# Optimization experiments

Measured on AMD Instinct MI355X. Metric: run time of the kernel, lower is better.

Reference implementation:

```python
import jax, jax.numpy as jnp
import numpy as np

# Complete 8-ary tree, depth 5 (levels 0..5), nodes stored level-major.
C = 8
DEPTH = 5
E = 64
H = 512
VOCAB = 20
SIZES = [C ** d for d in range(DEPTH + 1)]
OFFSETS = np.concatenate([[0], np.cumsum(SIZES)]).tolist()
TOTAL = OFFSETS[-1]  # 37449


def setup_inputs() -> dict:
    key = jax.random.key(0)
    ks = jax.random.split(key, 8)
    node_types = jax.random.randint(ks[0], (TOTAL,), 0, 19, dtype=jnp.int32)
    emb = jax.random.normal(ks[1], (VOCAB, E), jnp.float32)
    s_c = 1.0 / np.sqrt(E + H)
    s_g = 1.0 / np.sqrt(H)
    Wc_w = jax.random.normal(ks[2], (H, E + H), jnp.float32) * s_c
    Wc_b = jax.random.normal(ks[3], (H,), jnp.float32) * s_c
    W_ih = jax.random.normal(ks[4], (3 * H, H), jnp.float32) * s_g
    W_hh = jax.random.normal(ks[5], (3 * H, H), jnp.float32) * s_g
    b_ih = jax.random.normal(ks[6], (3 * H,), jnp.float32) * s_g
    b_hh = jax.random.normal(ks[7], (3 * H,), jnp.float32) * s_g
    return {"node_types": node_types, "emb": emb, "Wc_w": Wc_w, "Wc_b": Wc_b,
            "W_ih": W_ih, "W_hh": W_hh, "b_ih": b_ih, "b_hh": b_hh}


def _gru_last(seq, W_ih, W_hh, b_ih, b_hh):
    """PyTorch-convention GRU over child axis; seq: [n, C, H] -> last hidden [n, H]."""
    n = seq.shape[0]
    gx = jnp.einsum('ncH,gH->cng', seq, W_ih) + b_ih  # [C, n, 3H], precomputed input gates

    def step(h, gx_t):
        gh = h @ W_hh.T + b_hh
        xr, xz, xn = jnp.split(gx_t, 3, axis=-1)
        hr, hz, hn = jnp.split(gh, 3, axis=-1)
        r = jax.nn.sigmoid(xr + hr)
        z = jax.nn.sigmoid(xz + hz)
        cand = jnp.tanh(xn + r * hn)
        h_new = (1.0 - z) * cand + z * h
        return h_new, None

    h0 = jnp.zeros((n, H), seq.dtype)
    h_last, _ = jax.lax.scan(step, h0, gx)
    return h_last


def reference(node_types, emb, Wc_w, Wc_b, W_ih, W_hh, b_ih, b_hh):
    embeds = emb[node_types]                       # [TOTAL, E]
    Wc_e = Wc_w[:, :E]                              # acts on embedding part
    Wc_h = Wc_w[:, E:]                              # acts on child-encoding part
    # Leaf level: hidden part of concat is zero-padded -> only Wc_e contributes.
    off = OFFSETS[DEPTH]
    h = jnp.tanh(embeds[off:off + SIZES[DEPTH]] @ Wc_e.T + Wc_b)  # [8^5, H]
    # Bottom-up level batching: each internal node's children are contiguous.
    for d in range(DEPTH - 1, -1, -1):
        child_seq = h.reshape(SIZES[d], C, H)
        child_enc = _gru_last(child_seq, W_ih, W_hh, b_ih, b_hh)  # [8^d, H]
        off = OFFSETS[d]
        h = jnp.tanh(embeds[off:off + SIZES[d]] @ Wc_e.T + child_enc @ Wc_h.T + Wc_b)
    return h[0]  # root encoding, [H]
```

## Files before the change

kernel.cpp:

```cpp
#include <hip/hip_runtime.h>
#include <hip/hip_bf16.h>
#include <math.h>

#define HID 512
#define WCW_LD 576
#define LEAF 4681

typedef unsigned short u16;
typedef __attribute__((ext_vector_type(8))) short bf16x8;
typedef __attribute__((ext_vector_type(4))) float f32x4;

__device__ __forceinline__ u16 f2bf(float f) {
    union { float f; unsigned u; } x; x.f = f;
    unsigned r = x.u + 0x7fffu + ((x.u >> 16) & 1u);
    return (u16)(r >> 16);
}
__device__ __forceinline__ float bf2f(u16 b) {
    union { unsigned u; float f; } x; x.u = ((unsigned)b) << 16; return x.f;
}
__device__ __forceinline__ float sigm(float x) { return 1.f / (1.f + expf(-x)); }

__device__ __forceinline__ int swz(int row, int byte) { return byte ^ ((row & 7) << 4); }

__global__ void pe_kernel(const float* __restrict__ emb, const float* __restrict__ Wc_w,
                          const float* __restrict__ Wc_b, float* __restrict__ Pe,
                          u16* __restrict__ PeT16) {
    int v = blockIdx.x, j = threadIdx.x;
    __shared__ float e[64];
    if (threadIdx.x < 64) e[threadIdx.x] = emb[v * 64 + threadIdx.x];
    __syncthreads();
    float acc = Wc_b[j];
    const float* w = Wc_w + (long long)j * WCW_LD;
#pragma unroll 8
    for (int k = 0; k < 64; ++k) acc += e[k] * w[k];
    Pe[v * HID + j] = acc;
    PeT16[v * HID + j] = f2bf(tanhf(acc));
}

__global__ void conv_w_kernel(const float* __restrict__ W_ih, const float* __restrict__ W_hh,
                              const float* __restrict__ Wc_w,
                              u16* __restrict__ Wih16, u16* __restrict__ Whh16,
                              u16* __restrict__ Wch16) {
    int idx = blockIdx.x * blockDim.x + threadIdx.x;
    int stride = gridDim.x * blockDim.x;
    for (int i = idx; i < 3 * HID * HID; i += stride) {
        Wih16[i] = f2bf(W_ih[i]);
        Whh16[i] = f2bf(W_hh[i]);
    }
    for (int i = idx; i < HID * HID; i += stride) {
        int j = i >> 9, k = i & 511;
        Wch16[i] = f2bf(Wc_w[(long long)j * WCW_LD + 64 + k]);
    }
}

__global__ __launch_bounds__(256)
void gx20_kernel(const u16* __restrict__ PeT16, const u16* __restrict__ Wih16,
                 const float* __restrict__ b_ih, float* __restrict__ Gx20) {
    int v = blockIdx.x;
    int j = blockIdx.y * 256 + threadIdx.x;
    const u16* a = PeT16 + v * HID;
    const u16* b = Wih16 + (long long)j * HID;
    float acc = b_ih[j];
    for (int k = 0; k < HID; k += 8) {
        bf16x8 av = *(const bf16x8*)(a + k);
        bf16x8 bv = *(const bf16x8*)(b + k);
#pragma unroll
        for (int i = 0; i < 8; ++i) acc += bf2f((u16)av[i]) * bf2f((u16)bv[i]);
    }
    Gx20[v * 1536 + j] = acc;
}

__global__ void h1_kernel(const float* __restrict__ Gx20, const float* __restrict__ b_hh,
                          float* __restrict__ H1f, u16* __restrict__ H1_16) {
    int v = blockIdx.x, j = threadIdx.x;
    float xr = Gx20[v * 1536 + j], xz = Gx20[v * 1536 + 512 + j], xn = Gx20[v * 1536 + 1024 + j];
    float r = sigm(xr + b_hh[j]);
    float z = sigm(xz + b_hh[HID + j]);
    float cand = tanhf(xn + r * b_hh[2 * HID + j]);
    float h = (1.f - z) * cand;
    H1f[v * HID + j] = h;
    H1_16[v * HID + j] = f2bf(h);
}

__global__ __launch_bounds__(256)
void gx_gemm(const u16* __restrict__ Asrc, const u16* __restrict__ Wih16,
             const float* __restrict__ b_ih, u16* __restrict__ gx16, int M) {
    __shared__ __align__(16) uint8_t sA[128 * 128];
    __shared__ __align__(16) uint8_t sB[64 * 128];
    int tid = threadIdx.x, lane = tid & 63, w = tid >> 6;
    int j0 = blockIdx.x * 64;
    int m0 = blockIdx.y * 128;

    f32x4 acc[2][4];
#pragma unroll
    for (int m = 0; m < 2; ++m)
#pragma unroll
        for (int jf = 0; jf < 4; ++jf) acc[m][jf] = (f32x4){0.f, 0.f, 0.f, 0.f};

    for (int k0 = 0; k0 < HID; k0 += 64) {
#pragma unroll
        for (int l = 0; l < 4; ++l) {
            int e = tid + l * 256;
            int r = e >> 3, c = e & 7;
            int gm = m0 + r;
            uint4 v = make_uint4(0u, 0u, 0u, 0u);
            if (gm < M) v = *(const uint4*)(Asrc + (long long)gm * HID + k0 + c * 8);
            *(uint4*)(sA + r * 128 + swz(r, c * 16)) = v;
        }
#pragma unroll
        for (int l = 0; l < 2; ++l) {
            int e = tid + l * 256;
            int r = e >> 3, c = e & 7;
            uint4 v = *(const uint4*)(Wih16 + (long long)(j0 + r) * HID + k0 + c * 8);
            *(uint4*)(sB + r * 128 + swz(r, c * 16)) = v;
        }
        __syncthreads();
#pragma unroll
        for (int ks = 0; ks < 2; ++ks) {
            int kb = ks * 64 + ((lane >> 4) << 4);
            int ar = lane & 15;
            bf16x8 a0 = *(const bf16x8*)(sA + (w * 32 + ar) * 128 + swz(ar, kb));
            bf16x8 a1 = *(const bf16x8*)(sA + (w * 32 + 16 + ar) * 128 + swz(ar, kb));
#pragma unroll
            for (int jf = 0; jf < 4; ++jf) {
                bf16x8 b = *(const bf16x8*)(sB + (jf * 16 + ar) * 128 + swz(ar, kb));
                acc[0][jf] = __builtin_amdgcn_mfma_f32_16x16x32_bf16(a0, b, acc[0][jf], 0, 0, 0);
                acc[1][jf] = __builtin_amdgcn_mfma_f32_16x16x32_bf16(a1, b, acc[1][jf], 0, 0, 0);
            }
        }
        __syncthreads();
    }

#pragma unroll
    for (int jf = 0; jf < 4; ++jf) {
        int j = j0 + jf * 16 + (lane & 15);
        float bias = b_ih[j];
#pragma unroll
        for (int m = 0; m < 2; ++m) {
#pragma unroll
            for (int q = 0; q < 4; ++q) {
                int row = m0 + w * 32 + m * 16 + (lane >> 4) * 4 + q;
                if (row < M) gx16[(long long)row * 1536 + j] = f2bf(acc[m][jf][q] + bias);
            }
        }
    }
}

template<int GX_TABLE, int H_TABLE>
__global__ __launch_bounds__(256, 4)
void gru_step_h(const u16* __restrict__ hsrc16, const float* __restrict__ hsrc_f,
                const u16* __restrict__ H1_16, const float* __restrict__ H1f,
                const float* __restrict__ Gx20, const u16* __restrict__ gx16, int t,
                const int* __restrict__ nt,
                float* __restrict__ hdst_f, u16* __restrict__ hdst16,
                const u16* __restrict__ Whh16, const float* __restrict__ b_hh, int n) {
    __shared__ __align__(16) uint8_t sm[4][8192];
    int tid = threadIdx.x;
    int p0 = blockIdx.x * 64, j0 = blockIdx.y * 64;
    int lane = tid & 63, w = tid >> 6, wr = w >> 1, wc = w & 1;

    f32x4 acc[3][2][2];
#pragma unroll
    for (int g = 0; g < 3; ++g)
#pragma unroll
        for (int i = 0; i < 2; ++i)
#pragma unroll
            for (int j = 0; j < 2; ++j) acc[g][i][j] = (f32x4){0.f, 0.f, 0.f, 0.f};

    for (int kt = 0; kt < 8; ++kt) {
        int k0 = kt * 64;
#pragma unroll
        for (int l = 0; l < 2; ++l) {
            int e = tid + l * 256;
            int r = e >> 3, c = e & 7;
            int p = p0 + r;
            uint4 v = make_uint4(0u, 0u, 0u, 0u);
            if (p < n) {
                const u16* src = H_TABLE ? (H1_16 + (long long)nt[LEAF + p * 8] * HID)
                                         : (hsrc16 + (long long)p * HID);
                v = *(const uint4*)(src + k0 + c * 8);
            }
            *(uint4*)(sm[0] + r * 128 + swz(r, c * 16)) = v;
        }
#pragma unroll
        for (int g = 0; g < 3; ++g) {
#pragma unroll
            for (int l = 0; l < 2; ++l) {
                int e = tid + l * 256;
                int r = e >> 3, c = e & 7;
                uint4 v = *(const uint4*)(Whh16 + (long long)(g * HID + j0 + r) * HID + k0 + c * 8);
                *(uint4*)(sm[1 + g] + r * 128 + swz(r, c * 16)) = v;
            }
        }
        __syncthreads();
#pragma unroll
        for (int s = 0; s < 2; ++s) {
            int kb = s * 64 + ((lane >> 4) << 4);
            int ar = lane & 15;
            bf16x8 a0 = *(const bf16x8*)(sm[0] + (wr * 32 + ar) * 128 + swz(ar, kb));
            bf16x8 a1 = *(const bf16x8*)(sm[0] + (wr * 32 + 16 + ar) * 128 + swz(ar, kb));
#pragma unroll
            for (int g = 0; g < 3; ++g) {
#pragma unroll
                for (int jf = 0; jf < 2; ++jf) {
                    bf16x8 b = *(const bf16x8*)(sm[1 + g] + (wc * 32 + jf * 16 + ar) * 128 + swz(ar, kb));
                    acc[g][0][jf] = __builtin_amdgcn_mfma_f32_16x16x32_bf16(a0, b, acc[g][0][jf], 0, 0, 0);
                    acc[g][1][jf] = __builtin_amdgcn_mfma_f32_16x16x32_bf16(a1, b, acc[g][1][jf], 0, 0, 0);
                }
            }
        }
        __syncthreads();
    }

#pragma unroll
    for (int i = 0; i < 2; ++i) {
#pragma unroll
        for (int jf = 0; jf < 2; ++jf) {
            int jj = j0 + wc * 32 + jf * 16 + (lane & 15);
            float bhr = b_hh[jj], bhz = b_hh[HID + jj], bhn = b_hh[2 * HID + jj];
#pragma unroll
            for (int q = 0; q < 4; ++q) {
                int p = p0 + wr * 32 + i * 16 + (lane >> 4) * 4 + q;
                if (p >= n) continue;
                float xr, xz, xn;
                if (GX_TABLE) {
                    int v = nt[LEAF + p * 8 + t];
                    const float* gp = Gx20 + (long long)v * 1536 + jj;
                    xr = gp[0]; xz = gp[512]; xn = gp[1024];
                } else {
                    long long gb = ((long long)(p * 8 + t)) * 1536 + jj;
                    xr = bf2f(gx16[gb]); xz = bf2f(gx16[gb + 512]); xn = bf2f(gx16[gb + 1024]);
                }
                float hp = H_TABLE ? H1f[(long long)nt[LEAF + p * 8] * HID + jj]
                                   : hsrc_f[(long long)p * HID + jj];
                float r = sigm(xr + acc[0][i][jf][q] + bhr);
                float z = sigm(xz + acc[1][i][jf][q] + bhz);
                float cand = tanhf(xn + r * (acc[2][i][jf][q] + bhn));
                float hnew = (1.f - z) * cand + z * hp;
                hdst_f[(long long)p * HID + jj] = hnew;
                hdst16[(long long)p * HID + jj] = f2bf(hnew);
            }
        }
    }
}

__global__ __launch_bounds__(256, 4)
void combine_mfma(const u16* __restrict__ enc_in, const u16* __restrict__ Wch16,
                  const int* __restrict__ nt, int off, const float* __restrict__ Pe,
                  u16* __restrict__ out16, int n) {
    __shared__ __align__(16) uint8_t sm[2][8192];
    int tid = threadIdx.x;
    int p0 = blockIdx.x * 64, j0 = blockIdx.y * 64;
    int lane = tid & 63, w = tid >> 6, wr = w >> 1, wc = w & 1;

    f32x4 acc[2][2];
#pragma unroll
    for (int i = 0; i < 2; ++i)
#pragma unroll
        for (int j = 0; j < 2; ++j) acc[i][j] = (f32x4){0.f, 0.f, 0.f, 0.f};

    for (int kt = 0; kt < 8; ++kt) {
        int k0 = kt * 64;
#pragma unroll
        for (int l = 0; l < 2; ++l) {
            int e = tid + l * 256;
            int r = e >> 3, c = e & 7;
            uint4 v = make_uint4(0u, 0u, 0u, 0u);
            if (p0 + r < n) v = *(const uint4*)(enc_in + (long long)(p0 + r) * HID + k0 + c * 8);
            *(uint4*)(sm[0] + r * 128 + swz(r, c * 16)) = v;
        }
#pragma unroll
        for (int l = 0; l < 2; ++l) {
            int e = tid + l * 256;
            int r = e >> 3, c = e & 7;
            uint4 v = *(const uint4*)(Wch16 + (long long)(j0 + r) * HID + k0 + c * 8);
            *(uint4*)(sm[1] + r * 128 + swz(r, c * 16)) = v;
        }
        __syncthreads();
#pragma unroll
        for (int s = 0; s < 2; ++s) {
            int kb = s * 64 + ((lane >> 4) << 4);
            int ar = lane & 15;
            bf16x8 a0 = *(const bf16x8*)(sm[0] + (wr * 32 + ar) * 128 + swz(ar, kb));
            bf16x8 a1 = *(const bf16x8*)(sm[0] + (wr * 32 + 16 + ar) * 128 + swz(ar, kb));
#pragma unroll
            for (int j = 0; j < 2; ++j) {
                bf16x8 b = *(const bf16x8*)(sm[1] + (wc * 32 + j * 16 + ar) * 128 + swz(ar, kb));
                acc[0][j] = __builtin_amdgcn_mfma_f32_16x16x32_bf16(a0, b, acc[0][j], 0, 0, 0);
                acc[1][j] = __builtin_amdgcn_mfma_f32_16x16x32_bf16(a1, b, acc[1][j], 0, 0, 0);
            }
        }
        __syncthreads();
    }

#pragma unroll
    for (int i = 0; i < 2; ++i) {
#pragma unroll
        for (int j = 0; j < 2; ++j) {
            int jj = j0 + wc * 32 + j * 16 + (lane & 15);
#pragma unroll
            for (int q = 0; q < 4; ++q) {
                int p = p0 + wr * 32 + i * 16 + (lane >> 4) * 4 + q;
                if (p >= n) continue;
                int tv = nt[off + p];
                float v = tanhf(Pe[(long long)tv * HID + jj] + acc[i][j][q]);
                out16[(long long)p * HID + jj] = f2bf(v);
            }
        }
    }
}

__global__ __launch_bounds__(256)
void t0_simt(const u16* __restrict__ gx16, const float* __restrict__ b_hh,
             float* __restrict__ hdst_f, u16* __restrict__ hdst16, int n) {
    int idx = blockIdx.x * 256 + threadIdx.x;
    int p = idx >> 9, j = idx & 511;
    if (p >= n) return;
    long long gb = ((long long)(p * 8)) * 1536 + j;
    float xr = bf2f(gx16[gb]), xz = bf2f(gx16[gb + 512]), xn = bf2f(gx16[gb + 1024]);
    float r = sigm(xr + b_hh[j]);
    float z = sigm(xz + b_hh[HID + j]);
    float cand = tanhf(xn + r * b_hh[2 * HID + j]);
    float h = (1.f - z) * cand;
    hdst_f[(long long)p * HID + j] = h;
    hdst16[(long long)p * HID + j] = f2bf(h);
}

__global__ __launch_bounds__(256)
void step_simt(const u16* __restrict__ gx16, int t,
               const float* __restrict__ hsrc_f, const u16* __restrict__ hsrc16,
               float* __restrict__ hdst_f, u16* __restrict__ hdst16,
               const u16* __restrict__ Whh16, const float* __restrict__ b_hh, int n) {
    int idx = blockIdx.x * 256 + threadIdx.x;
    int kc = idx & 3, pj = idx >> 2;
    int p = pj >> 9, j = pj & 511;
    if (p >= n) return;
    const u16* hp16 = hsrc16 + (long long)p * HID + kc * 128;
    const u16* w0 = Whh16 + (long long)j * HID + kc * 128;
    const u16* w1 = w0 + (long long)HID * HID;
    const u16* w2 = w1 + (long long)HID * HID;
    float a0 = 0.f, a1 = 0.f, a2 = 0.f;
#pragma unroll 4
    for (int k = 0; k < 128; k += 8) {
        bf16x8 hv = *(const bf16x8*)(hp16 + k);
        bf16x8 v0 = *(const bf16x8*)(w0 + k);
        bf16x8 v1 = *(const bf16x8*)(w1 + k);
        bf16x8 v2 = *(const bf16x8*)(w2 + k);
#pragma unroll
        for (int i = 0; i < 8; ++i) {
            float hh = bf2f((u16)hv[i]);
            a0 += hh * bf2f((u16)v0[i]);
            a1 += hh * bf2f((u16)v1[i]);
            a2 += hh * bf2f((u16)v2[i]);
        }
    }
    a0 += __shfl_xor(a0, 1); a0 += __shfl_xor(a0, 2);
    a1 += __shfl_xor(a1, 1); a1 += __shfl_xor(a1, 2);
    a2 += __shfl_xor(a2, 1); a2 += __shfl_xor(a2, 2);
    if (kc == 0) {
        long long gb = ((long long)(p * 8 + t)) * 1536 + j;
        float xr = bf2f(gx16[gb]), xz = bf2f(gx16[gb + 512]), xn = bf2f(gx16[gb + 1024]);
        float r = sigm(xr + a0 + b_hh[j]);
        float z = sigm(xz + a1 + b_hh[HID + j]);
        float cand = tanhf(xn + r * (a2 + b_hh[2 * HID + j]));
        float hp = hsrc_f[(long long)p * HID + j];
        float hnew = (1.f - z) * cand + z * hp;
        hdst_f[(long long)p * HID + j] = hnew;
        hdst16[(long long)p * HID + j] = f2bf(hnew);
    }
}

__global__ __launch_bounds__(256)
void combine_simt(const u16* __restrict__ h16, const u16* __restrict__ Wch16,
                  const int* __restrict__ nt, int off, const float* __restrict__ Pe,
                  u16* __restrict__ enc16, float* __restrict__ outf, int n) {
    int idx = blockIdx.x * 256 + threadIdx.x;
    int kc = idx & 3, pj = idx >> 2;
    int p = pj >> 9, j = pj & 511;
    if (p >= n) return;
    const u16* hp = h16 + (long long)p * HID + kc * 128;
    const u16* wr = Wch16 + (long long)j * HID + kc * 128;
    float a = 0.f;
#pragma unroll 4
    for (int k = 0; k < 128; k += 8) {
        bf16x8 hv = *(const bf16x8*)(hp + k);
        bf16x8 wv = *(const bf16x8*)(wr + k);
#pragma unroll
        for (int i = 0; i < 8; ++i) a += bf2f((u16)hv[i]) * bf2f((u16)wv[i]);
    }
    a += __shfl_xor(a, 1); a += __shfl_xor(a, 2);
    if (kc == 0) {
        int tv = nt[off + p];
        float v = tanhf(Pe[(long long)tv * HID + j] + a);
        enc16[(long long)p * HID + j] = f2bf(v);
        if (outf) outf[(long long)p * HID + j] = v;
    }
}

extern "C" void kernel_launch(void* const* d_in, const int* in_sizes, int n_in,
                              void* d_out, int out_size, void* d_ws, size_t ws_size,
                              hipStream_t stream) {
    const int*   nt   = (const int*)d_in[0];
    const float* emb  = (const float*)d_in[1];
    const float* Wc_w = (const float*)d_in[2];
    const float* Wc_b = (const float*)d_in[3];
    const float* W_ih = (const float*)d_in[4];
    const float* W_hh = (const float*)d_in[5];
    const float* b_ih = (const float*)d_in[6];
    const float* b_hh = (const float*)d_in[7];

    uint8_t* p = (uint8_t*)d_ws;
    u16*   gx16  = (u16*)p;   p += (size_t)4096 * 1536 * 2;
    u16*   enc16 = (u16*)p;   p += (size_t)4096 * HID * 2;
    float* hf[2]; u16* h16[2];
    hf[0]  = (float*)p; p += (size_t)4096 * HID * 4;
    hf[1]  = (float*)p; p += (size_t)4096 * HID * 4;
    h16[0] = (u16*)p;   p += (size_t)4096 * HID * 2;
    h16[1] = (u16*)p;   p += (size_t)4096 * HID * 2;
    u16*   Wih16 = (u16*)p;   p += (size_t)3 * HID * HID * 2;
    u16*   Whh16 = (u16*)p;   p += (size_t)3 * HID * HID * 2;
    u16*   Wch16 = (u16*)p;   p += (size_t)HID * HID * 2;
    float* Pe    = (float*)p; p += (size_t)20 * HID * 4;
    u16*   PeT16 = (u16*)p;   p += (size_t)20 * HID * 2;
    float* Gx20  = (float*)p; p += (size_t)20 * 1536 * 4;
    float* H1f   = (float*)p; p += (size_t)20 * HID * 4;
    u16*   H1_16 = (u16*)p;   p += (size_t)20 * HID * 2;

    conv_w_kernel<<<1024, 256, 0, stream>>>(W_ih, W_hh, Wc_w, Wih16, Whh16, Wch16);
    pe_kernel<<<20, 512, 0, stream>>>(emb, Wc_w, Wc_b, Pe, PeT16);
    gx20_kernel<<<dim3(20, 6), 256, 0, stream>>>(PeT16, Wih16, b_ih, Gx20);
    h1_kernel<<<20, 512, 0, stream>>>(Gx20, b_hh, H1f, H1_16);

    {
        int n = 4096;
        dim3 sgrid(n / 64, 8);
        gru_step_h<1, 1><<<sgrid, 256, 0, stream>>>(nullptr, nullptr, H1_16, H1f,
                                                    Gx20, nullptr, 1, nt,
                                                    hf[0], h16[0], Whh16, b_hh, n);
        int cur = 0;
        for (int t = 2; t < 8; ++t) {
            gru_step_h<1, 0><<<sgrid, 256, 0, stream>>>(h16[cur], hf[cur], nullptr, nullptr,
                                                        Gx20, nullptr, t, nt,
                                                        hf[cur ^ 1], h16[cur ^ 1], Whh16, b_hh, n);
            cur ^= 1;
        }
        combine_mfma<<<sgrid, 256, 0, stream>>>(h16[cur], Wch16, nt, 585, Pe, enc16, n);
    }

    const int sizes[4] = {512, 64, 8, 1};
    const int offs[4]  = {73, 9, 1, 0};
    for (int li = 0; li < 4; ++li) {
        int n = sizes[li], off = offs[li];
        int M = n * 8;
        dim3 ggrid(24, (M + 127) / 128);
        gx_gemm<<<ggrid, 256, 0, stream>>>(enc16, Wih16, b_ih, gx16, M);

        t0_simt<<<n * 2, 256, 0, stream>>>(gx16, b_hh, hf[0], h16[0], n);
        int cur = 0;
        if (n >= 512) {
            dim3 sgrid(n / 64, 8);
            for (int t = 1; t < 8; ++t) {
                gru_step_h<0, 0><<<sgrid, 256, 0, stream>>>(h16[cur], hf[cur], nullptr, nullptr,
                                                            nullptr, gx16, t, nt,
                                                            hf[cur ^ 1], h16[cur ^ 1], Whh16, b_hh, n);
                cur ^= 1;
            }
            combine_mfma<<<sgrid, 256, 0, stream>>>(h16[cur], Wch16, nt, off, Pe, enc16, n);
        } else {
            for (int t = 1; t < 8; ++t) {
                step_simt<<<n * 8, 256, 0, stream>>>(gx16, t, hf[cur], h16[cur],
                                                     hf[cur ^ 1], h16[cur ^ 1], Whh16, b_hh, n);
                cur ^= 1;
            }
            combine_simt<<<n * 8, 256, 0, stream>>>(h16[cur], Wch16, nt, off, Pe, enc16,
                                                    (li == 3) ? (float*)d_out : (float*)0, n);
        }
    }
}
```

Baseline: 684.1 us.

## Tabulate leaf GRU steps over vocabulary pairs and use 128-row step tiles

Leaf tokens take only 20 values, so hidden states after steps 1 and 2 depend only on the first one or two tokens. These are precomputed as 20- and 400-row tables via a small GEMM and expanded per node, replacing two full 4096-row recurrent GEMM launches. The remaining leaf steps use a new kernel with 128-row tiles for more weight reuse per block. This adds extra small kernels and larger register use in the new step kernel.

```diff
diff --git a/kernel.cpp b/kernel.cpp
--- a/kernel.cpp
+++ b/kernel.cpp
@@ -82,9 +82,11 @@
     H1_16[v * HID + j] = f2bf(h);
 }
 
-__global__ __launch_bounds__(256)
-void gx_gemm(const u16* __restrict__ Asrc, const u16* __restrict__ Wih16,
-             const float* __restrict__ b_ih, u16* __restrict__ gx16, int M) {
+template<bool F32OUT>
+__global__ __launch_bounds__(256)
+void gx_gemm(const u16* __restrict__ Asrc, const u16* __restrict__ W16,
+             const float* __restrict__ bias, u16* __restrict__ g16,
+             float* __restrict__ gf, int M) {
     __shared__ __align__(16) uint8_t sA[128 * 128];
     __shared__ __align__(16) uint8_t sB[64 * 128];
     int tid = threadIdx.x, lane = tid & 63, w = tid >> 6;
@@ -111,7 +113,7 @@
         for (int l = 0; l < 2; ++l) {
             int e = tid + l * 256;
             int r = e >> 3, c = e & 7;
-            uint4 v = *(const uint4*)(Wih16 + (long long)(j0 + r) * HID + k0 + c * 8);
+            uint4 v = *(const uint4*)(W16 + (long long)(j0 + r) * HID + k0 + c * 8);
             *(uint4*)(sB + r * 128 + swz(r, c * 16)) = v;
         }
         __syncthreads();
@@ -134,24 +136,142 @@
 #pragma unroll
     for (int jf = 0; jf < 4; ++jf) {
         int j = j0 + jf * 16 + (lane & 15);
-        float bias = b_ih[j];
+        float bv = bias[j];
 #pragma unroll
         for (int m = 0; m < 2; ++m) {
 #pragma unroll
             for (int q = 0; q < 4; ++q) {
                 int row = m0 + w * 32 + m * 16 + (lane >> 4) * 4 + q;
-                if (row < M) gx16[(long long)row * 1536 + j] = f2bf(acc[m][jf][q] + bias);
-            }
-        }
-    }
-}
-
-template<int GX_TABLE, int H_TABLE>
+                if (row < M) {
+                    float val = acc[m][jf][q] + bv;
+                    if (F32OUT) gf[(long long)row * 1536 + j] = val;
+                    else        g16[(long long)row * 1536 + j] = f2bf(val);
+                }
+            }
+        }
+    }
+}
+
+__global__ __launch_bounds__(256)
+void h2_expand(const float* __restrict__ Gx20, const float* __restrict__ Gh1,
+               const float* __restrict__ H1f, float* __restrict__ h2f,
+               u16* __restrict__ h2_16) {
+    int idx = blockIdx.x * 256 + threadIdx.x;
+    int pr = idx >> 9, j = idx & 511;
+    int v0 = pr / 20, v1 = pr % 20;
+    const float* gx = Gx20 + (long long)v1 * 1536 + j;
+    const float* gh = Gh1 + (long long)v0 * 1536 + j;
+    float r = sigm(gx[0] + gh[0]);
+    float z = sigm(gx[512] + gh[512]);
+    float cand = tanhf(gx[1024] + r * gh[1024]);
+    float h = (1.f - z) * cand + z * H1f[(long long)v0 * HID + j];
+    h2f[(long long)pr * HID + j] = h;
+    h2_16[(long long)pr * HID + j] = f2bf(h);
+}
+
+__global__ __launch_bounds__(256)
+void h3_expand(const float* __restrict__ Gx20, const float* __restrict__ Gh2,
+               const float* __restrict__ h2f, const int* __restrict__ nt,
+               float* __restrict__ hdst_f, u16* __restrict__ hdst16) {
+    int idx = blockIdx.x * 256 + threadIdx.x;
+    int p = idx >> 9, j = idx & 511;
+    int v0 = nt[LEAF + p * 8], v1 = nt[LEAF + p * 8 + 1], v2 = nt[LEAF + p * 8 + 2];
+    int pr = v0 * 20 + v1;
+    const float* gx = Gx20 + (long long)v2 * 1536 + j;
+    const float* gh = Gh2 + (long long)pr * 1536 + j;
+    float r = sigm(gx[0] + gh[0]);
+    float z = sigm(gx[512] + gh[512]);
+    float cand = tanhf(gx[1024] + r * gh[1024]);
+    float h = (1.f - z) * cand + z * h2f[(long long)pr * HID + j];
+    hdst_f[(long long)p * HID + j] = h;
+    hdst16[(long long)p * HID + j] = f2bf(h);
+}
+
+__global__ __launch_bounds__(256)
+void step128_l4(const u16* __restrict__ hsrc16, const float* __restrict__ hsrc_f,
+                const float* __restrict__ Gx20, int t, const int* __restrict__ nt,
+                float* __restrict__ hdst_f, u16* __restrict__ hdst16,
+                const u16* __restrict__ Whh16, const float* __restrict__ b_hh, int n) {
+    __shared__ __align__(16) uint8_t sA[128 * 128];
+    __shared__ __align__(16) uint8_t sB[3][64 * 128];
+    int tid = threadIdx.x, lane = tid & 63, w = tid >> 6;
+    int m0 = blockIdx.x * 128, j0 = blockIdx.y * 64;
+
+    f32x4 acc[3][2][4];
+#pragma unroll
+    for (int g = 0; g < 3; ++g)
+#pragma unroll
+        for (int m = 0; m < 2; ++m)
+#pragma unroll
+            for (int jf = 0; jf < 4; ++jf) acc[g][m][jf] = (f32x4){0.f, 0.f, 0.f, 0.f};
+
+    for (int k0 = 0; k0 < HID; k0 += 64) {
+#pragma unroll
+        for (int l = 0; l < 4; ++l) {
+            int e = tid + l * 256;
+            int r = e >> 3, c = e & 7;
+            int gm = m0 + r;
+            uint4 v = make_uint4(0u, 0u, 0u, 0u);
+            if (gm < n) v = *(const uint4*)(hsrc16 + (long long)gm * HID + k0 + c * 8);
+            *(uint4*)(sA + r * 128 + swz(r, c * 16)) = v;
+        }
+#pragma unroll
+        for (int g = 0; g < 3; ++g) {
+#pragma unroll
+            for (int l = 0; l < 2; ++l) {
+                int e = tid + l * 256;
+                int r = e >> 3, c = e & 7;
+                uint4 v = *(const uint4*)(Whh16 + (long long)(g * HID + j0 + r) * HID + k0 + c * 8);
+                *(uint4*)(sB[g] + r * 128 + swz(r, c * 16)) = v;
+            }
+        }
+        __syncthreads();
+#pragma unroll
+        for (int ks = 0; ks < 2; ++ks) {
+            int kb = ks * 64 + ((lane >> 4) << 4);
+            int ar = lane & 15;
+            bf16x8 a0 = *(const bf16x8*)(sA + (w * 32 + ar) * 128 + swz(ar, kb));
+            bf16x8 a1 = *(const bf16x8*)(sA + (w * 32 + 16 + ar) * 128 + swz(ar, kb));
+#pragma unroll
+            for (int g = 0; g < 3; ++g) {
+#pragma unroll
+                for (int jf = 0; jf < 4; ++jf) {
+                    bf16x8 b = *(const bf16x8*)(sB[g] + (jf * 16 + ar) * 128 + swz(ar, kb));
+                    acc[g][0][jf] = __builtin_amdgcn_mfma_f32_16x16x32_bf16(a0, b, acc[g][0][jf], 0, 0, 0);
+                    acc[g][1][jf] = __builtin_amdgcn_mfma_f32_16x16x32_bf16(a1, b, acc[g][1][jf], 0, 0, 0);
+                }
+            }
+        }
+        __syncthreads();
+    }
+
+#pragma unroll
+    for (int jf = 0; jf < 4; ++jf) {
+        int jj = j0 + jf * 16 + (lane & 15);
+        float bhr = b_hh[jj], bhz = b_hh[HID + jj], bhn = b_hh[2 * HID + jj];
+#pragma unroll
+        for (int m = 0; m < 2; ++m) {
+#pragma unroll
+            for (int q = 0; q < 4; ++q) {
+                int p = m0 + w * 32 + m * 16 + (lane >> 4) * 4 + q;
+                if (p >= n) continue;
+                int v = nt[LEAF + p * 8 + t];
+                const float* gp = Gx20 + (long long)v * 1536 + jj;
+                float r = sigm(gp[0] + acc[0][m][jf][q] + bhr);
+                float z = sigm(gp[512] + acc[1][m][jf][q] + bhz);
+                float cand = tanhf(gp[1024] + r * (acc[2][m][jf][q] + bhn));
+                float hp = hsrc_f[(long long)p * HID + jj];
+                float hnew = (1.f - z) * cand + z * hp;
+                hdst_f[(long long)p * HID + jj] = hnew;
+                hdst16[(long long)p * HID + jj] = f2bf(hnew);
+            }
+        }
+    }
+}
+
 __global__ __launch_bounds__(256, 4)
 void gru_step_h(const u16* __restrict__ hsrc16, const float* __restrict__ hsrc_f,
-                const u16* __restrict__ H1_16, const float* __restrict__ H1f,
-                const float* __restrict__ Gx20, const u16* __restrict__ gx16, int t,
-                const int* __restrict__ nt,
+                const u16* __restrict__ gx16, int t,
                 float* __restrict__ hdst_f, u16* __restrict__ hdst16,
                 const u16* __restrict__ Whh16, const float* __restrict__ b_hh, int n) {
     __shared__ __align__(16) uint8_t sm[4][8192];
@@ -175,11 +295,7 @@
             int r = e >> 3, c = e & 7;
             int p = p0 + r;
             uint4 v = make_uint4(0u, 0u, 0u, 0u);
-            if (p < n) {
-                const u16* src = H_TABLE ? (H1_16 + (long long)nt[LEAF + p * 8] * HID)
-                                         : (hsrc16 + (long long)p * HID);
-                v = *(const uint4*)(src + k0 + c * 8);
-            }
+            if (p < n) v = *(const uint4*)(hsrc16 + (long long)p * HID + k0 + c * 8);
             *(uint4*)(sm[0] + r * 128 + swz(r, c * 16)) = v;
         }
 #pragma unroll
@@ -222,20 +338,12 @@
             for (int q = 0; q < 4; ++q) {
                 int p = p0 + wr * 32 + i * 16 + (lane >> 4) * 4 + q;
                 if (p >= n) continue;
-                float xr, xz, xn;
-                if (GX_TABLE) {
-                    int v = nt[LEAF + p * 8 + t];
-                    const float* gp = Gx20 + (long long)v * 1536 + jj;
-                    xr = gp[0]; xz = gp[512]; xn = gp[1024];
-                } else {
-                    long long gb = ((long long)(p * 8 + t)) * 1536 + jj;
-                    xr = bf2f(gx16[gb]); xz = bf2f(gx16[gb + 512]); xn = bf2f(gx16[gb + 1024]);
-                }
-                float hp = H_TABLE ? H1f[(long long)nt[LEAF + p * 8] * HID + jj]
-                                   : hsrc_f[(long long)p * HID + jj];
+                long long gb = ((long long)(p * 8 + t)) * 1536 + jj;
+                float xr = bf2f(gx16[gb]), xz = bf2f(gx16[gb + 512]), xn = bf2f(gx16[gb + 1024]);
                 float r = sigm(xr + acc[0][i][jf][q] + bhr);
                 float z = sigm(xz + acc[1][i][jf][q] + bhz);
                 float cand = tanhf(xn + r * (acc[2][i][jf][q] + bhn));
+                float hp = hsrc_f[(long long)p * HID + jj];
                 float hnew = (1.f - z) * cand + z * hp;
                 hdst_f[(long long)p * HID + jj] = hnew;
                 hdst16[(long long)p * HID + jj] = f2bf(hnew);
@@ -425,6 +533,10 @@
     float* Gx20  = (float*)p; p += (size_t)20 * 1536 * 4;
     float* H1f   = (float*)p; p += (size_t)20 * HID * 4;
     u16*   H1_16 = (u16*)p;   p += (size_t)20 * HID * 2;
+    float* Gh1   = (float*)p; p += (size_t)20 * 1536 * 4;
+    float* Gh2   = (float*)p; p += (size_t)400 * 1536 * 4;
+    float* h2f   = (float*)p; p += (size_t)400 * HID * 4;
+    u16*   h2_16 = (u16*)p;   p += (size_t)400 * HID * 2;
 
     conv_w_kernel<<<1024, 256, 0, stream>>>(W_ih, W_hh, Wc_w, Wih16, Whh16, Wch16);
     pe_kernel<<<20, 512, 0, stream>>>(emb, Wc_w, Wc_b, Pe, PeT16);
@@ -433,18 +545,19 @@
 
     {
         int n = 4096;
-        dim3 sgrid(n / 64, 8);
-        gru_step_h<1, 1><<<sgrid, 256, 0, stream>>>(nullptr, nullptr, H1_16, H1f,
-                                                    Gx20, nullptr, 1, nt,
-                                                    hf[0], h16[0], Whh16, b_hh, n);
+        gx_gemm<true><<<dim3(24, 1), 256, 0, stream>>>(H1_16, Whh16, b_hh, nullptr, Gh1, 20);
+        h2_expand<<<800, 256, 0, stream>>>(Gx20, Gh1, H1f, h2f, h2_16);
+        gx_gemm<true><<<dim3(24, 4), 256, 0, stream>>>(h2_16, Whh16, b_hh, nullptr, Gh2, 400);
+        h3_expand<<<8192, 256, 0, stream>>>(Gx20, Gh2, h2f, nt, hf[0], h16[0]);
         int cur = 0;
-        for (int t = 2; t < 8; ++t) {
-            gru_step_h<1, 0><<<sgrid, 256, 0, stream>>>(h16[cur], hf[cur], nullptr, nullptr,
-                                                        Gx20, nullptr, t, nt,
-                                                        hf[cur ^ 1], h16[cur ^ 1], Whh16, b_hh, n);
+        dim3 sgrid(n / 128, 8);
+        for (int t = 3; t < 8; ++t) {
+            step128_l4<<<sgrid, 256, 0, stream>>>(h16[cur], hf[cur], Gx20, t, nt,
+                                                  hf[cur ^ 1], h16[cur ^ 1], Whh16, b_hh, n);
             cur ^= 1;
         }
-        combine_mfma<<<sgrid, 256, 0, stream>>>(h16[cur], Wch16, nt, 585, Pe, enc16, n);
+        dim3 cgrid(n / 64, 8);
+        combine_mfma<<<cgrid, 256, 0, stream>>>(h16[cur], Wch16, nt, 585, Pe, enc16, n);
     }
 
     const int sizes[4] = {512, 64, 8, 1};
@@ -453,16 +566,15 @@
         int n = sizes[li], off = offs[li];
         int M = n * 8;
         dim3 ggrid(24, (M + 127) / 128);
-        gx_gemm<<<ggrid, 256, 0, stream>>>(enc16, Wih16, b_ih, gx16, M);
+        gx_gemm<false><<<ggrid, 256, 0, stream>>>(enc16, Wih16, b_ih, gx16, nullptr, M);
 
         t0_simt<<<n * 2, 256, 0, stream>>>(gx16, b_hh, hf[0], h16[0], n);
         int cur = 0;
         if (n >= 512) {
             dim3 sgrid(n / 64, 8);
             for (int t = 1; t < 8; ++t) {
-                gru_step_h<0, 0><<<sgrid, 256, 0, stream>>>(h16[cur], hf[cur], nullptr, nullptr,
-                                                            nullptr, gx16, t, nt,
-                                                            hf[cur ^ 1], h16[cur ^ 1], Whh16, b_hh, n);
+                gru_step_h<<<sgrid, 256, 0, stream>>>(h16[cur], hf[cur], gx16, t,
+                                                      hf[cur ^ 1], h16[cur ^ 1], Whh16, b_hh, n);
                 cur ^= 1;
             }
             combine_mfma<<<sgrid, 256, 0, stream>>>(h16[cur], Wch16, nt, off, Pe, enc16, n);
```

After: 762.7 us. 1.11x slower.
